# Performance work log

Measured on AMD Instinct MI355X. Metric: run time of the kernel, lower is better.

Reference implementation:

```python
import jax, jax.numpy as jnp
import numpy as np

B, F = 8192, 256
H1, H2, H3 = 32, 64, 32
ORDER = 2
OUT = 1


def setup_inputs() -> dict:
    key = jax.random.key(0)
    ks = jax.random.split(key, 6)
    x = jax.random.normal(ks[0], (B, F), dtype=jnp.float32)
    # stacked per-feature FeatureNet weights, fan-in scaled to keep ReLUs active
    W1 = jax.random.normal(ks[1], (F, 1, H1), dtype=jnp.float32) * 1.0
    b1 = jnp.zeros((F, H1), dtype=jnp.float32)
    W2 = jax.random.normal(ks[2], (F, H1, H2), dtype=jnp.float32) * (1.0 / np.sqrt(H1))
    b2 = jnp.zeros((F, H2), dtype=jnp.float32)
    W3 = jax.random.normal(ks[3], (F, H2, H3), dtype=jnp.float32) * (1.0 / np.sqrt(H2))
    b3 = jnp.zeros((F, H3), dtype=jnp.float32)
    Wout = jax.random.normal(ks[4], (ORDER * H3, OUT), dtype=jnp.float32) * (1.0 / np.sqrt(ORDER * H3))
    bout = jnp.zeros((OUT,), dtype=jnp.float32)
    return {"x": x, "W1": W1, "b1": b1, "W2": W2, "b2": b2,
            "W3": W3, "b3": b3, "Wout": Wout, "bout": bout}


def _feature_nets(x, W1, b1, W2, b2, W3, b3):
    # x: [B, F] -> per-feature tiny MLP 1->32->64->32, batched over F
    h = jax.nn.relu(x[:, :, None] * W1[:, 0, :][None] + b1[None])      # [B, F, 32]
    h = jax.nn.relu(jnp.einsum('bfh,fho->bfo', h, W2) + b2[None])       # [B, F, 64]
    h = jax.nn.relu(jnp.einsum('bfh,fho->bfo', h, W3) + b3[None])       # [B, F, 32]
    return h


def reference(x, W1, b1, W2, b2, W3, b3, Wout, bout):
    t = _feature_nets(x, W1, b1, W2, b2, W3, b3)  # [B, F, H3]
    # Newton's identity power-sum recurrence over interaction order
    p1 = t.sum(axis=1)                            # [B, H3]
    powers = [None, p1]                           # powers[0] unused (scalar 1 in orig)
    inters = [jnp.ones_like(p1), p1]              # interactions[0] = 1 (broadcast)
    for i in range(2, ORDER + 1):
        powers.append(jnp.power(t, i).sum(axis=1))
        cur = 0.0
        for j in range(1, i + 1):
            cur = cur + ((-1.0) ** (j + 1)) * powers[j] * inters[i - j]
        inters.append(cur / i)
    feats = jnp.concatenate(inters[1:], axis=1)   # [B, ORDER*H3]
    pred = feats @ Wout + bout                    # [B, OUT]
    return pred
```

## Files before the change

kernel.cpp:

```cpp
#include <hip/hip_runtime.h>
#include <hip/hip_bf16.h>

#define B_   8192
#define F_   256
#define NFC  8
#define NF   (F_/NFC)
#define NPH  (NF/2)
#define RPB  128
#define NSUB 2

typedef __attribute__((ext_vector_type(8))) short v8s;
typedef __attribute__((ext_vector_type(4))) float v4f;
typedef __attribute__((ext_vector_type(2))) float v2f;
typedef __attribute__((ext_vector_type(4))) unsigned int v4u;

static __device__ __forceinline__ unsigned short f2bf(float f) {
    __hip_bfloat16 h = __float2bfloat16(f);
    return __builtin_bit_cast(unsigned short, h);
}

static __device__ __forceinline__ unsigned cvtpk(float a, float b) {
    unsigned r;
    asm("v_cvt_pk_bf16_f32 %0, %1, %2" : "=v"(r) : "v"(a), "v"(b));
    return r;
}
static __device__ __forceinline__ v2f pk_add(v2f a, v2f b) {
    v2f d; asm("v_pk_add_f32 %0, %1, %2" : "=v"(d) : "v"(a), "v"(b)); return d;
}
static __device__ __forceinline__ v2f pk_fma(v2f a, v2f b, v2f c) {
    v2f d; asm("v_pk_fma_f32 %0, %1, %2, %3" : "=v"(d) : "v"(a), "v"(b), "v"(c)); return d;
}

static __device__ __forceinline__ void gload_lds16(const void* g, void* l) {
    __builtin_amdgcn_global_load_lds(
        (const __attribute__((address_space(1))) unsigned int*)g,
        (__attribute__((address_space(3))) unsigned int*)l,
        16, 0, 0);
}

__global__ __launch_bounds__(256)
void honam_prep(const float* __restrict__ w2g, const float* __restrict__ w3g,
                const float* __restrict__ w1g, const float* __restrict__ b1g,
                const float* __restrict__ b2g, const float* __restrict__ b3g,
                unsigned short* __restrict__ wf, float* __restrict__ pp)
{
    const int f   = blockIdx.x;
    const int tid = threadIdx.x;
    const float* w2 = w2g + (size_t)f * 2048;
    const float* w3 = w3g + (size_t)f * 2048;
    unsigned short* dst = wf + (size_t)f * 4096;
    for (int i = tid; i < 4096; i += 256) {
        const int frag = i >> 9;
        const int l    = (i >> 3) & 63;
        const int j    = i & 7;
        const int c    = l & 15;
        const int g    = l >> 4;
        float v;
        if (frag < 4) {
            v = w2[(g * 8 + j) * 64 + frag * 16 + c];
        } else {
            const int kk = (frag - 4) >> 1;
            const int n2 = (frag - 4) & 1;
            const int u  = (kk * 2 + (j >> 2)) * 16 + g * 4 + (j & 3);
            v = w3[u * 32 + n2 * 16 + c];
        }
        dst[i] = f2bf(v);
    }
    if (tid < 160) {
        float v;
        if (tid < 32)       v = w1g[f * 32 + tid];
        else if (tid < 64)  v = b1g[f * 32 + (tid - 32)];
        else if (tid < 128) v = b2g[f * 64 + (tid - 64)];
        else                v = b3g[f * 32 + (tid - 128)];
        pp[(size_t)f * 160 + tid] = v;
    }
}

__global__ __launch_bounds__(256, 2)
void honam_k1(const float* __restrict__ xg,
              const unsigned short* __restrict__ wfg, const float* __restrict__ ppg,
              float* __restrict__ p1part, float* __restrict__ p2part)
{
    __shared__ float xs[NF][RPB];
    __shared__ float ps[NF * 160];
    __shared__ short wbuf[2][2][4096] __attribute__((aligned(16)));

    const int tid  = threadIdx.x;
    const int wave = tid >> 6;
    const int lane = tid & 63;
    const int c16  = lane & 15;
    const int g4   = lane >> 4;

    const int bx = blockIdx.x;
    const int rb = bx >> 3;
    const int fc = bx & 7;
    const int r0 = rb * RPB;
    const int f0 = fc * NF;

    {
        const int rr = tid >> 2;
        const int q  = tid & 3;
#pragma unroll
        for (int p = 0; p < 2; ++p) {
            const int row = p * 64 + rr;
            const float4 va = *(const float4*)&xg[(size_t)(r0 + row) * F_ + f0 + q * 8];
            const float4 vb = *(const float4*)&xg[(size_t)(r0 + row) * F_ + f0 + q * 8 + 4];
            const int fb = q * 8;
            xs[fb + 0][row] = va.x; xs[fb + 1][row] = va.y;
            xs[fb + 2][row] = va.z; xs[fb + 3][row] = va.w;
            xs[fb + 4][row] = vb.x; xs[fb + 5][row] = vb.y;
            xs[fb + 6][row] = vb.z; xs[fb + 7][row] = vb.w;
        }
    }
    {
        const float4* src = (const float4*)(ppg + (size_t)f0 * 160);
        float4* dst = (float4*)ps;
#pragma unroll
        for (int p = 0; p < 5; ++p)
            dst[tid + p * 256] = src[tid + p * 256];
    }

    auto stage = [&](int set, int fp, int fl) {
        const char* src = (const char*)wfg + (size_t)(f0 + fl) * 8192
                        + (2 * wave) * 1024 + lane * 16;
        gload_lds16(src,        &wbuf[set][fp][(2 * wave) * 512]);
        gload_lds16(src + 1024, &wbuf[set][fp][(2 * wave + 1) * 512]);
    };

    stage(0, 0, 0);
    stage(0, 1, 1);
    __syncthreads();

    v2f pacc1[NSUB][2][2];
    v2f pacc2[NSUB][2][2];
#pragma unroll
    for (int s = 0; s < NSUB; ++s)
#pragma unroll
        for (int n2 = 0; n2 < 2; ++n2)
#pragma unroll
            for (int jp = 0; jp < 2; ++jp) {
                pacc1[s][n2][jp] = (v2f){0.f, 0.f};
                pacc2[s][n2][jp] = (v2f){0.f, 0.f};
            }

    auto computeFeat = [&](int set, int fp, int fl) {
        const short* wb = &wbuf[set][fp][0];
        v8s wfr[8];
#pragma unroll
        for (int fr = 0; fr < 8; ++fr)
            wfr[fr] = *(const v8s*)&wb[fr * 512 + lane * 8];

        const int fb = fl * 160;
        const float4 w1a = *(const float4*)&ps[fb + g4 * 8];
        const float4 w1b = *(const float4*)&ps[fb + g4 * 8 + 4];
        const float4 b1a = *(const float4*)&ps[fb + 32 + g4 * 8];
        const float4 b1b = *(const float4*)&ps[fb + 32 + g4 * 8 + 4];
        const float w1v[8] = {w1a.x, w1a.y, w1a.z, w1a.w, w1b.x, w1b.y, w1b.z, w1b.w};
        const float b1v[8] = {b1a.x, b1a.y, b1a.z, b1a.w, b1b.x, b1b.y, b1b.z, b1b.w};
        v4f b2cv[4];
#pragma unroll
        for (int n = 0; n < 4; ++n)
            b2cv[n] = *(const v4f*)&ps[fb + 64 + n * 16 + g4 * 4];
        float b3v[2];
#pragma unroll
        for (int n = 0; n < 2; ++n) b3v[n] = ps[fb + 128 + n * 16 + c16];

        float xm[NSUB];
#pragma unroll
        for (int s = 0; s < NSUB; ++s)
            xm[s] = xs[fl][s * 64 + wave * 16 + c16];

#pragma unroll
        for (int sub = 0; sub < NSUB; ++sub) {
            unsigned h1p[4];
#pragma unroll
            for (int jj = 0; jj < 4; ++jj) {
                const float e0 = fmaxf(fmaf(xm[sub], w1v[2 * jj],     b1v[2 * jj]),     0.f);
                const float e1 = fmaxf(fmaf(xm[sub], w1v[2 * jj + 1], b1v[2 * jj + 1]), 0.f);
                h1p[jj] = cvtpk(e0, e1);
            }
            const v8s bh1 = __builtin_bit_cast(v8s, (v4u){h1p[0], h1p[1], h1p[2], h1p[3]});

            __builtin_amdgcn_s_setprio(1);
            v4f acc2[4];
#pragma unroll
            for (int n = 0; n < 4; ++n)
                acc2[n] = __builtin_amdgcn_mfma_f32_16x16x32_bf16(wfr[n], bh1, b2cv[n], 0, 0, 0);
            __builtin_amdgcn_s_setprio(0);

            unsigned q[8];
#pragma unroll
            for (int n = 0; n < 4; ++n) {
                q[2 * n]     = cvtpk(fmaxf(acc2[n][0], 0.f), fmaxf(acc2[n][1], 0.f));
                q[2 * n + 1] = cvtpk(fmaxf(acc2[n][2], 0.f), fmaxf(acc2[n][3], 0.f));
            }
            const v8s a2k0 = __builtin_bit_cast(v8s, (v4u){q[0], q[1], q[2], q[3]});
            const v8s a2k1 = __builtin_bit_cast(v8s, (v4u){q[4], q[5], q[6], q[7]});

            __builtin_amdgcn_s_setprio(1);
            v4f acc3[2];
#pragma unroll
            for (int n2 = 0; n2 < 2; ++n2) {
                acc3[n2] = __builtin_amdgcn_mfma_f32_16x16x32_bf16(
                    a2k0, wfr[4 + n2], (v4f){b3v[n2], b3v[n2], b3v[n2], b3v[n2]}, 0, 0, 0);
                acc3[n2] = __builtin_amdgcn_mfma_f32_16x16x32_bf16(
                    a2k1, wfr[6 + n2], acc3[n2], 0, 0, 0);
            }
            __builtin_amdgcn_s_setprio(0);
#pragma unroll
            for (int n2 = 0; n2 < 2; ++n2)
#pragma unroll
                for (int jp = 0; jp < 2; ++jp) {
                    v2f t;
                    t.x = fmaxf(acc3[n2][2 * jp],     0.f);
                    t.y = fmaxf(acc3[n2][2 * jp + 1], 0.f);
                    pacc1[sub][n2][jp] = pk_add(pacc1[sub][n2][jp], t);
                    pacc2[sub][n2][jp] = pk_fma(t, t, pacc2[sub][n2][jp]);
                }
        }
    };

    for (int ph = 0; ph < NPH; ++ph) {
        const int set = ph & 1;
        if (ph + 1 < NPH) {
            stage(set ^ 1, 0, 2 * ph + 2);
            stage(set ^ 1, 1, 2 * ph + 3);
        }
        computeFeat(set, 0, 2 * ph);
        computeFeat(set, 1, 2 * ph + 1);
        __syncthreads();
    }

    float* p1c = p1part + (size_t)fc * (B_ * 32);
    float* p2c = p2part + (size_t)fc * (B_ * 32);
#pragma unroll
    for (int sub = 0; sub < NSUB; ++sub)
#pragma unroll
        for (int n2 = 0; n2 < 2; ++n2)
#pragma unroll
            for (int jp = 0; jp < 2; ++jp) {
                const int row = r0 + sub * 64 + wave * 16 + g4 * 4 + 2 * jp;
                const int col = n2 * 16 + c16;
                p1c[row * 32 + col]       = pacc1[sub][n2][jp].x;
                p1c[(row + 1) * 32 + col] = pacc1[sub][n2][jp].y;
                p2c[row * 32 + col]       = pacc2[sub][n2][jp].x;
                p2c[(row + 1) * 32 + col] = pacc2[sub][n2][jp].y;
            }
}

__global__ __launch_bounds__(256)
void honam_k2(const float* __restrict__ p1part, const float* __restrict__ p2part,
              const float* __restrict__ woutg, const float* __restrict__ boutg,
              float* __restrict__ outg)
{
    const int tid = threadIdx.x;
    const int o   = tid & 31;
    const int r   = blockIdx.x * 8 + (tid >> 5);
    const size_t idx = (size_t)r * 32 + o;

    float s1 = 0.f, s2 = 0.f;
#pragma unroll
    for (int fc = 0; fc < NFC; ++fc) {
        s1 += p1part[(size_t)fc * (B_ * 32) + idx];
        s2 += p2part[(size_t)fc * (B_ * 32) + idx];
    }
    const float wa = woutg[o];
    const float wb = woutg[32 + o];
    float val = s1 * wa + 0.5f * (s1 * s1 - s2) * wb;
#pragma unroll
    for (int off = 16; off > 0; off >>= 1)
        val += __shfl_down(val, off, 32);
    if (o == 0) outg[r] = val + boutg[0];
}

extern "C" void kernel_launch(void* const* d_in, const int* in_sizes, int n_in,
                              void* d_out, int out_size, void* d_ws, size_t ws_size,
                              hipStream_t stream)
{
    const float* xg    = (const float*)d_in[0];
    const float* w1g   = (const float*)d_in[1];
    const float* b1g   = (const float*)d_in[2];
    const float* w2g   = (const float*)d_in[3];
    const float* b2g   = (const float*)d_in[4];
    const float* w3g   = (const float*)d_in[5];
    const float* b3g   = (const float*)d_in[6];
    const float* woutg = (const float*)d_in[7];
    const float* boutg = (const float*)d_in[8];
    float* outg = (float*)d_out;

    float* p1part = (float*)d_ws;
    float* p2part = p1part + (size_t)NFC * B_ * 32;
    unsigned short* wf = (unsigned short*)(p2part + (size_t)NFC * B_ * 32);
    float* pp = (float*)(wf + (size_t)F_ * 4096);

    honam_prep<<<dim3(F_), dim3(256), 0, stream>>>(w2g, w3g, w1g, b1g, b2g, b3g, wf, pp);

    honam_k1<<<dim3((B_ / RPB) * NFC), dim3(256), 0, stream>>>(
        xg, wf, pp, p1part, p2part);

    honam_k2<<<dim3(B_ / 8), dim3(256), 0, stream>>>(p1part, p2part, woutg, boutg, outg);
}
```

Measured before the change: 57.17 us.

## Split features into 16 chunks, raise occupancy, pack layer-1 FMAs, drop setprio

Doubles the number of feature chunks per row block so the grid has twice as many blocks, each handling 16 features, and asks for three blocks per CU through launch bounds. The x and parameter staging loads are adjusted to the smaller chunk, layer-1 is computed with packed FMAs, the s_setprio hints around the MFMAs are removed, and the phase loop is unrolled by two. More blocks and occupancy aim to hide latency better. The cost is twice as many partial-sum writes for the reduction kernel and possible register pressure from the occupancy target.

```diff
diff --git a/kernel.cpp b/kernel.cpp
--- a/kernel.cpp
+++ b/kernel.cpp
@@ -3,7 +3,7 @@
 
 #define B_   8192
 #define F_   256
-#define NFC  8
+#define NFC  16
 #define NF   (F_/NFC)
 #define NPH  (NF/2)
 #define RPB  128
@@ -76,7 +76,7 @@
     }
 }
 
-__global__ __launch_bounds__(256, 2)
+__global__ __launch_bounds__(256, 3)
 void honam_k1(const float* __restrict__ xg,
               const unsigned short* __restrict__ wfg, const float* __restrict__ ppg,
               float* __restrict__ p1part, float* __restrict__ p2part)
@@ -92,32 +92,28 @@
     const int g4   = lane >> 4;
 
     const int bx = blockIdx.x;
-    const int rb = bx >> 3;
-    const int fc = bx & 7;
+    const int rb = bx >> 4;
+    const int fc = bx & 15;
     const int r0 = rb * RPB;
     const int f0 = fc * NF;
 
     {
-        const int rr = tid >> 2;
-        const int q  = tid & 3;
-#pragma unroll
-        for (int p = 0; p < 2; ++p) {
-            const int row = p * 64 + rr;
-            const float4 va = *(const float4*)&xg[(size_t)(r0 + row) * F_ + f0 + q * 8];
-            const float4 vb = *(const float4*)&xg[(size_t)(r0 + row) * F_ + f0 + q * 8 + 4];
-            const int fb = q * 8;
-            xs[fb + 0][row] = va.x; xs[fb + 1][row] = va.y;
-            xs[fb + 2][row] = va.z; xs[fb + 3][row] = va.w;
-            xs[fb + 4][row] = vb.x; xs[fb + 5][row] = vb.y;
-            xs[fb + 6][row] = vb.z; xs[fb + 7][row] = vb.w;
-        }
+        const int row  = tid >> 1;
+        const int half = tid & 1;
+        const float4 va = *(const float4*)&xg[(size_t)(r0 + row) * F_ + f0 + half * 8];
+        const float4 vb = *(const float4*)&xg[(size_t)(r0 + row) * F_ + f0 + half * 8 + 4];
+        const int fb = half * 8;
+        xs[fb + 0][row] = va.x; xs[fb + 1][row] = va.y;
+        xs[fb + 2][row] = va.z; xs[fb + 3][row] = va.w;
+        xs[fb + 4][row] = vb.x; xs[fb + 5][row] = vb.y;
+        xs[fb + 6][row] = vb.z; xs[fb + 7][row] = vb.w;
     }
     {
         const float4* src = (const float4*)(ppg + (size_t)f0 * 160);
         float4* dst = (float4*)ps;
-#pragma unroll
-        for (int p = 0; p < 5; ++p)
-            dst[tid + p * 256] = src[tid + p * 256];
+        dst[tid]       = src[tid];
+        dst[tid + 256] = src[tid + 256];
+        if (tid < 128) dst[tid + 512] = src[tid + 512];
     }
 
     auto stage = [&](int set, int fp, int fl) {
@@ -151,12 +147,12 @@
             wfr[fr] = *(const v8s*)&wb[fr * 512 + lane * 8];
 
         const int fb = fl * 160;
-        const float4 w1a = *(const float4*)&ps[fb + g4 * 8];
-        const float4 w1b = *(const float4*)&ps[fb + g4 * 8 + 4];
-        const float4 b1a = *(const float4*)&ps[fb + 32 + g4 * 8];
-        const float4 b1b = *(const float4*)&ps[fb + 32 + g4 * 8 + 4];
-        const float w1v[8] = {w1a.x, w1a.y, w1a.z, w1a.w, w1b.x, w1b.y, w1b.z, w1b.w};
-        const float b1v[8] = {b1a.x, b1a.y, b1a.z, b1a.w, b1b.x, b1b.y, b1b.z, b1b.w};
+        v2f w1p[4], b1p[4];
+#pragma unroll
+        for (int p = 0; p < 4; ++p) {
+            w1p[p] = *(const v2f*)&ps[fb + g4 * 8 + 2 * p];
+            b1p[p] = *(const v2f*)&ps[fb + 32 + g4 * 8 + 2 * p];
+        }
         v4f b2cv[4];
 #pragma unroll
         for (int n = 0; n < 4; ++n)
@@ -172,21 +168,19 @@
 
 #pragma unroll
         for (int sub = 0; sub < NSUB; ++sub) {
+            const v2f xp = (v2f){xm[sub], xm[sub]};
             unsigned h1p[4];
 #pragma unroll
             for (int jj = 0; jj < 4; ++jj) {
-                const float e0 = fmaxf(fmaf(xm[sub], w1v[2 * jj],     b1v[2 * jj]),     0.f);
-                const float e1 = fmaxf(fmaf(xm[sub], w1v[2 * jj + 1], b1v[2 * jj + 1]), 0.f);
-                h1p[jj] = cvtpk(e0, e1);
+                const v2f e = pk_fma(xp, w1p[jj], b1p[jj]);
+                h1p[jj] = cvtpk(fmaxf(e.x, 0.f), fmaxf(e.y, 0.f));
             }
             const v8s bh1 = __builtin_bit_cast(v8s, (v4u){h1p[0], h1p[1], h1p[2], h1p[3]});
 
-            __builtin_amdgcn_s_setprio(1);
             v4f acc2[4];
 #pragma unroll
             for (int n = 0; n < 4; ++n)
                 acc2[n] = __builtin_amdgcn_mfma_f32_16x16x32_bf16(wfr[n], bh1, b2cv[n], 0, 0, 0);
-            __builtin_amdgcn_s_setprio(0);
 
             unsigned q[8];
 #pragma unroll
@@ -197,7 +191,6 @@
             const v8s a2k0 = __builtin_bit_cast(v8s, (v4u){q[0], q[1], q[2], q[3]});
             const v8s a2k1 = __builtin_bit_cast(v8s, (v4u){q[4], q[5], q[6], q[7]});
 
-            __builtin_amdgcn_s_setprio(1);
             v4f acc3[2];
 #pragma unroll
             for (int n2 = 0; n2 < 2; ++n2) {
@@ -206,7 +199,6 @@
                 acc3[n2] = __builtin_amdgcn_mfma_f32_16x16x32_bf16(
                     a2k1, wfr[6 + n2], acc3[n2], 0, 0, 0);
             }
-            __builtin_amdgcn_s_setprio(0);
 #pragma unroll
             for (int n2 = 0; n2 < 2; ++n2)
 #pragma unroll
@@ -220,6 +212,7 @@
         }
     };
 
+#pragma unroll 2
     for (int ph = 0; ph < NPH; ++ph) {
         const int set = ph & 1;
         if (ph + 1 < NPH) {
```

Result: faster. 52.37 us (-8.4%).
